# Optimization experiments

Hardware: AMD Instinct MI355X
Metric: run time of the kernel (lower is better)

The kernel has to match this reference:

```python
import jax, jax.numpy as jnp
import numpy as np

N, D_TOK, K = 8192, 256, 16


def knn_idx(xyz, k):
    # squared pairwise distances, diagonal excluded (loop=False)
    sq = jnp.sum(xyz * xyz, axis=-1)                      # [N]
    dist = sq[:, None] - 2.0 * (xyz @ xyz.T) + sq[None, :]  # [N,N]
    dist = dist + jnp.eye(xyz.shape[0], dtype=xyz.dtype) * jnp.asarray(1e10, xyz.dtype)
    _, idx = jax.lax.top_k(-dist, k)                      # [N,k] nearest neighbors j for each target i
    return idx


def edgeconv(x, nbr, W1, b1, W2, b2):
    # EdgeConv message: nn(concat(x_i, x_j - x_i)), aggr = max over neighbors
    n, d = x.shape
    k = nbr.shape[1]
    xi = x[:, None, :]                                    # [N,1,D]
    xj = x[nbr]                                           # [N,k,D] gather
    msg = jnp.concatenate([jnp.broadcast_to(xi, (n, k, d)), xj - xi], axis=-1)  # [N,k,2D]
    h = jax.nn.relu(msg @ W1 + b1) @ W2 + b2              # [N,k,token_dim]
    return jnp.max(h, axis=1)                             # [N,token_dim]


def setup_inputs() -> dict:
    key = jax.random.key(0)
    ks = jax.random.split(key, 10)
    d_in = 2 * (D_TOK + 3)
    s1 = 1.0 / np.sqrt(d_in)
    s2 = 1.0 / np.sqrt(D_TOK)
    return {
        "xyz": jax.random.normal(ks[0], (N, 3), dtype=jnp.float32),
        "feat": jax.random.normal(ks[1], (N, D_TOK), dtype=jnp.float32),
        "W1a": jax.random.normal(ks[2], (d_in, D_TOK), dtype=jnp.float32) * s1,
        "b1a": jnp.zeros((D_TOK,), dtype=jnp.float32),
        "W2a": jax.random.normal(ks[3], (D_TOK, D_TOK), dtype=jnp.float32) * s2,
        "b2a": jnp.zeros((D_TOK,), dtype=jnp.float32),
        "W1b": jax.random.normal(ks[4], (d_in, D_TOK), dtype=jnp.float32) * s1,
        "b1b": jnp.zeros((D_TOK,), dtype=jnp.float32),
        "W2b": jax.random.normal(ks[5], (D_TOK, D_TOK), dtype=jnp.float32) * s2,
        "b2b": jnp.zeros((D_TOK,), dtype=jnp.float32),
    }


def reference(xyz, feat, W1a, b1a, W2a, b2a, W1b, b1b, W2b, b2b):
    nbr = knn_idx(xyz, K)                                 # [N,k], built once, reused by both convs
    x = jnp.concatenate([feat, xyz], axis=-1)             # [N, D_TOK+3]
    x = edgeconv(x, nbr, W1a, b1a, W2a, b2a)              # [N, D_TOK]
    x = jnp.concatenate([x, xyz], axis=-1)                # [N, D_TOK+3]
    x = edgeconv(x, nbr, W1b, b1b, W2b, b2b)              # [N, D_TOK]
    return x
```

## Files before the change

kernel.cpp:

```cpp
#include <hip/hip_runtime.h>
#include <cfloat>

#define N_PTS 8192
#define DTOK 256
#define KNN 16

typedef __attribute__((ext_vector_type(8))) short short8;
typedef __attribute__((ext_vector_type(4))) float float4v;

__device__ inline short f2bf(float f) {
  unsigned u = __float_as_uint(f);
  u += 0x7fffu + ((u >> 16) & 1u);
  return (short)(u >> 16);
}
__device__ inline float bf2f(short h) {
  return __uint_as_float(((unsigned)(unsigned short)h) << 16);
}

__global__ __launch_bounds__(256) void knn_prep_kernel(
    const float* __restrict__ xyz, float4* __restrict__ xyz4) {
  const int i = blockIdx.x * 256 + threadIdx.x;
  float x = xyz[3 * i], y = xyz[3 * i + 1], z = xyz[3 * i + 2];
  float sq = __fadd_rn(__fadd_rn(__fmul_rn(x, x), __fmul_rn(y, y)),
                       __fmul_rn(z, z));
  xyz4[i] = make_float4(x, y, z, sq);
}

__device__ inline float cand_dist(const float4 p, float xi, float yi, float zi,
                                  float sqi, int j, int i) {
  const float dot = fmaf(zi, p.z, fmaf(yi, p.y, __fmul_rn(xi, p.x)));
  float d = __fadd_rn(__fsub_rn(sqi, __fmul_rn(2.0f, dot)), p.w);
  if (j == i) d = __fadd_rn(d, 1e10f);
  return d;
}

#define KCH 512
#define NCH (N_PTS / KCH)

__global__ __launch_bounds__(256) void knn_select_kernel(
    const float4* __restrict__ xyz4, int* __restrict__ nbr) {
  __shared__ float4 cs[2][KCH];
  const int tid = threadIdx.x;
  const int lane = tid & 63;
  const int wave = tid >> 6;
  const int i = blockIdx.x * 4 + wave;

  const float4 pi = xyz4[i];
  const float xi = pi.x, yi = pi.y, zi = pi.z, sqi = pi.w;

  float4 p0 = xyz4[tid];
  float4 p1 = xyz4[tid + 256];
  cs[0][tid] = p0;
  cs[0][tid + 256] = p1;
  __syncthreads();

  float lmin0 = FLT_MAX, lmin1 = FLT_MAX;
  for (int c = 0; c < NCH; ++c) {
    const int b = c & 1;
    if (c < NCH - 1) {
      p0 = xyz4[(c + 1) * KCH + tid];
      p1 = xyz4[(c + 1) * KCH + tid + 256];
    }
    const int base = c * KCH;
    #pragma unroll
    for (int s = 0; s < 8; s += 2) {
      const float4 q0 = cs[b][s * 64 + lane];
      const float4 q1 = cs[b][(s + 1) * 64 + lane];
      lmin0 = fminf(lmin0, cand_dist(q0, xi, yi, zi, sqi,
                                     base + s * 64 + lane, i));
      lmin1 = fminf(lmin1, cand_dist(q1, xi, yi, zi, sqi,
                                     base + (s + 1) * 64 + lane, i));
    }
    if (c < NCH - 1) {
      cs[b ^ 1][tid] = p0;
      cs[b ^ 1][tid + 256] = p1;
    }
    __syncthreads();
  }
  const float lmin = fminf(lmin0, lmin1);

  float v = lmin;
  #pragma unroll
  for (int k = 2; k <= 64; k <<= 1) {
    #pragma unroll
    for (int j = k >> 1; j > 0; j >>= 1) {
      const float o = __shfl_xor(v, j, 64);
      const bool up = ((lane & k) == 0);
      const bool lo = ((lane & j) == 0);
      v = (up == lo) ? fminf(v, o) : fmaxf(v, o);
    }
  }
  const float t = __shfl(v, 15, 64);

  float sd = FLT_MAX;
  int sj = 0;
  float s15 = FLT_MAX;

  p0 = xyz4[tid];
  p1 = xyz4[tid + 256];
  cs[0][tid] = p0;
  cs[0][tid + 256] = p1;
  __syncthreads();

  for (int c = 0; c < NCH; ++c) {
    const int b = c & 1;
    if (c < NCH - 1) {
      p0 = xyz4[(c + 1) * KCH + tid];
      p1 = xyz4[(c + 1) * KCH + tid + 256];
    }
    const int cbase = c * KCH;

    float dd[8];
    #pragma unroll
    for (int s = 0; s < 8; ++s) {
      const float4 q = cs[b][s * 64 + lane];
      dd[s] = cand_dist(q, xi, yi, zi, sqi, cbase + s * 64 + lane, i);
    }

    #pragma unroll
    for (int s = 0; s < 8; ++s) {
      unsigned long long m = __ballot((dd[s] < s15) && (dd[s] <= t));
      const int base = cbase + s * 64;
      while (m) {
        const int src = __ffsll(m) - 1;
        m &= m - 1;
        const float dc = __shfl(dd[s], src);
        if (dc < s15) {
          const int jc = base + src;
          const unsigned long long bm = __ballot(sd <= dc) & 0xFFFFull;
          const int pos = (int)__popcll(bm);
          const float pu = __shfl_up(sd, 1);
          const int ju = __shfl_up(sj, 1);
          if (lane < 16) {
            if (lane > pos)        { sd = pu; sj = ju; }
            else if (lane == pos)  { sd = dc; sj = jc; }
          }
          s15 = __shfl(sd, 15);
        }
      }
    }

    if (c < NCH - 1) {
      cs[b ^ 1][tid] = p0;
      cs[b ^ 1][tid + 256] = p1;
    }
    __syncthreads();
  }
  if (lane < 16) nbr[i * KNN + lane] = sj;
}

__global__ __launch_bounds__(256) void convert_w_kernel(
    const float* __restrict__ W1, short* __restrict__ bhi,
    short* __restrict__ blo) {
  const int n = blockIdx.x;
  const int k = threadIdx.x;
  const float v = (n < 256) ? W1[k * DTOK + n]
                            : W1[(259 + k) * DTOK + (n - 256)];
  short h = f2bf(v);
  bhi[n * 256 + k] = h;
  blo[n * 256 + k] = f2bf(v - bf2f(h));
}

__global__ __launch_bounds__(256, 2) void pq_gemm_fused_kernel(
    const float* __restrict__ A, const short* __restrict__ Bthi,
    const short* __restrict__ Btlo, const float* __restrict__ xyz,
    const float* __restrict__ W1, const float* __restrict__ b1,
    float* __restrict__ R, float* __restrict__ Q) {
  __shared__ short Ahi[64][32], Alo[64][32];
  __shared__ short Bhi[128][32], Blo[128][32];
  __shared__ float Qs[64][65];
  __shared__ float sx[64][3];
  __shared__ float swz[6][64];
  __shared__ float sb1[64];

  const int tid = threadIdx.x;
  const int lane = tid & 63;
  const int wave = tid >> 6;
  const int l15 = lane & 15;
  const int quad = lane >> 4;
  const int mh = wave & 1;
  const int qh = wave >> 1;
  const int m0 = blockIdx.x * 64;
  const int np0 = blockIdx.y * 64;

  if (tid < 64) {
    sx[tid][0] = xyz[(m0 + tid) * 3];
    sx[tid][1] = xyz[(m0 + tid) * 3 + 1];
    sx[tid][2] = xyz[(m0 + tid) * 3 + 2];
  } else if (tid < 128) {
    int n = tid - 64;
    sb1[n] = b1[np0 + n];
    #pragma unroll
    for (int r = 0; r < 3; ++r) {
      swz[r][n] = W1[(256 + r) * DTOK + np0 + n];
      swz[3 + r][n] = W1[(515 + r) * DTOK + np0 + n];
    }
  }

  float4v acc[2][4];
  #pragma unroll
  for (int mf = 0; mf < 2; ++mf)
    #pragma unroll
    for (int nf = 0; nf < 4; ++nf)
      #pragma unroll
      for (int e = 0; e < 4; ++e) acc[mf][nf][e] = 0.f;

  const int ar = tid >> 2;
  const int ak = (tid & 3) * 8;

  #pragma unroll 1
  for (int kc = 0; kc < 8; ++kc) {
    const int k0 = kc * 32;
    __syncthreads();
    {
      const float* asrc = A + (size_t)(m0 + ar) * 256 + k0 + ak;
      float4 a0 = *(const float4*)asrc;
      float4 a1 = *(const float4*)(asrc + 4);
      float v[8] = {a0.x, a0.y, a0.z, a0.w, a1.x, a1.y, a1.z, a1.w};
      short8 h8, l8;
      #pragma unroll
      for (int e = 0; e < 8; ++e) {
        short h = f2bf(v[e]);
        h8[e] = h;
        l8[e] = f2bf(v[e] - bf2f(h));
      }
      *(short8*)(&Ahi[ar][ak]) = h8;
      *(short8*)(&Alo[ar][ak]) = l8;
    }
    #pragma unroll
    for (int l = 0; l < 4; ++l) {
      const int rem = tid + 256 * (l & 1);
      const int row = rem >> 2;
      const int koff = (rem & 3) * 8;
      const int n = (row < 64) ? (np0 + row) : (256 + np0 + row - 64);
      const short* src = ((l < 2) ? Bthi : Btlo) + (size_t)n * 256 + k0 + koff;
      short8 vv = *(const short8*)src;
      if (l < 2) *(short8*)(&Bhi[row][koff]) = vv;
      else       *(short8*)(&Blo[row][koff]) = vv;
    }
    __syncthreads();

    short8 ah[2], al[2], bh[4], bl[4];
    #pragma unroll
    for (int mf = 0; mf < 2; ++mf) {
      ah[mf] = *(const short8*)(&Ahi[mh * 32 + mf * 16 + l15][quad * 8]);
      al[mf] = *(const short8*)(&Alo[mh * 32 + mf * 16 + l15][quad * 8]);
    }
    #pragma unroll
    for (int nf = 0; nf < 4; ++nf) {
      bh[nf] = *(const short8*)(&Bhi[qh * 64 + nf * 16 + l15][quad * 8]);
      bl[nf] = *(const short8*)(&Blo[qh * 64 + nf * 16 + l15][quad * 8]);
    }
    #pragma unroll
    for (int mf = 0; mf < 2; ++mf)
      #pragma unroll
      for (int nf = 0; nf < 4; ++nf) {
        acc[mf][nf] = __builtin_amdgcn_mfma_f32_16x16x32_bf16(
            ah[mf], bh[nf], acc[mf][nf], 0, 0, 0);
        acc[mf][nf] = __builtin_amdgcn_mfma_f32_16x16x32_bf16(
            ah[mf], bl[nf], acc[mf][nf], 0, 0, 0);
        acc[mf][nf] = __builtin_amdgcn_mfma_f32_16x16x32_bf16(
            al[mf], bh[nf], acc[mf][nf], 0, 0, 0);
      }
  }

  if (qh == 1) {
    #pragma unroll
    for (int mf = 0; mf < 2; ++mf)
      #pragma unroll
      for (int nf = 0; nf < 4; ++nf)
        #pragma unroll
        for (int e = 0; e < 4; ++e) {
          int row = mh * 32 + mf * 16 + quad * 4 + e;
          int col = nf * 16 + l15;
          float q = acc[mf][nf][e] + sx[row][0] * swz[3][col] +
                    sx[row][1] * swz[4][col] + sx[row][2] * swz[5][col];
          Qs[row][col] = q;
          Q[(size_t)(m0 + row) * DTOK + np0 + col] = q;
        }
  }
  __syncthreads();
  if (qh == 0) {
    #pragma unroll
    for (int mf = 0; mf < 2; ++mf)
      #pragma unroll
      for (int nf = 0; nf < 4; ++nf)
        #pragma unroll
        for (int e = 0; e < 4; ++e) {
          int row = mh * 32 + mf * 16 + quad * 4 + e;
          int col = nf * 16 + l15;
          float p = acc[mf][nf][e] + sx[row][0] * swz[0][col] +
                    sx[row][1] * swz[1][col] + sx[row][2] * swz[2][col];
          R[(size_t)(m0 + row) * DTOK + np0 + col] =
              (p + sb1[col]) - Qs[row][col];
        }
  }
}

#define EP 8

__global__ __launch_bounds__(256, 2) void edge_mfma_kernel(
    const float* __restrict__ R, const float* __restrict__ Q,
    const int* __restrict__ nbr, const float* __restrict__ W2,
    const float* __restrict__ b2, float* __restrict__ out,
    int num_groups, int groups_per_block) {
  __shared__ short Hs[EP * KNN * DTOK];
  const int lane = threadIdx.x & 63;
  const int wave = threadIdx.x >> 6;
  const int l15 = lane & 15;
  const int quad = lane >> 4;

  short8 bfr[4][8];
  #pragma unroll
  for (int nt_i = 0; nt_i < 4; ++nt_i) {
    const int n = (wave * 4 + nt_i) * 16 + l15;
    #pragma unroll
    for (int kt = 0; kt < 8; ++kt) {
      short8 f;
      #pragma unroll
      for (int jj = 0; jj < 8; ++jj) {
        int k = kt * 32 + quad * 8 + jj;
        f[jj] = f2bf(W2[k * DTOK + n]);
      }
      bfr[nt_i][kt] = f;
    }
  }

  const int wc8 = lane >> 1;
  const int wsub = (lane & 1) * 4;

  for (int gi = 0; gi < groups_per_block; ++gi) {
    const int g = blockIdx.x + gi * gridDim.x;
    if (g >= num_groups) break;
    const int i0 = g * EP;

    {
      const int ia = i0 + wave * 2;
      const int jr0 = nbr[ia * KNN + l15];
      const int jr1 = nbr[(ia + 1) * KNN + l15];
      const float4 ri0 = ((const float4*)(R + (size_t)ia * DTOK))[lane];
      const float4 ri1 = ((const float4*)(R + (size_t)(ia + 1) * DTOK))[lane];
      #pragma unroll
      for (int pp = 0; pp < 2; ++pp) {
        const float4 ri = pp ? ri1 : ri0;
        const int jr = pp ? jr1 : jr0;
        #pragma unroll
        for (int k = 0; k < KNN; ++k) {
          const int j = __shfl(jr, k, 16);
          const float4 qj = ((const float4*)(Q + (size_t)j * DTOK))[lane];
          const int r = wave * 32 + pp * 16 + k;
          uint2 pk;
          pk.x = ((unsigned)(unsigned short)f2bf(fmaxf(ri.x + qj.x, 0.f))) |
                 (((unsigned)(unsigned short)f2bf(fmaxf(ri.y + qj.y, 0.f))) << 16);
          pk.y = ((unsigned)(unsigned short)f2bf(fmaxf(ri.z + qj.z, 0.f))) |
                 (((unsigned)(unsigned short)f2bf(fmaxf(ri.w + qj.w, 0.f))) << 16);
          *(uint2*)(&Hs[r * DTOK + ((wc8 ^ (r & 7)) << 3) + wsub]) = pk;
        }
      }
    }
    __syncthreads();

    #pragma unroll
    for (int mp = 0; mp < 4; ++mp) {
      float4v acc[2][4];
      #pragma unroll
      for (int mi = 0; mi < 2; ++mi)
        #pragma unroll
        for (int nt_i = 0; nt_i < 4; ++nt_i)
          #pragma unroll
          for (int e = 0; e < 4; ++e) acc[mi][nt_i][e] = 0.f;

      #pragma unroll
      for (int kt = 0; kt < 8; ++kt) {
        const int pc = ((kt * 4 + quad) ^ (l15 & 7)) << 3;
        const short8 a0 = *(const short8*)(
            &Hs[((mp * 2 + 0) * 16 + l15) * DTOK + pc]);
        const short8 a1 = *(const short8*)(
            &Hs[((mp * 2 + 1) * 16 + l15) * DTOK + pc]);
        #pragma unroll
        for (int nt_i = 0; nt_i < 4; ++nt_i) {
          acc[0][nt_i] = __builtin_amdgcn_mfma_f32_16x16x32_bf16(
              a0, bfr[nt_i][kt], acc[0][nt_i], 0, 0, 0);
          acc[1][nt_i] = __builtin_amdgcn_mfma_f32_16x16x32_bf16(
              a1, bfr[nt_i][kt], acc[1][nt_i], 0, 0, 0);
        }
      }

      #pragma unroll
      for (int mi = 0; mi < 2; ++mi) {
        #pragma unroll
        for (int nt_i = 0; nt_i < 4; ++nt_i) {
          float rm = fmaxf(fmaxf(acc[mi][nt_i][0], acc[mi][nt_i][1]),
                           fmaxf(acc[mi][nt_i][2], acc[mi][nt_i][3]));
          rm = fmaxf(rm, __shfl_xor(rm, 16, 64));
          rm = fmaxf(rm, __shfl_xor(rm, 32, 64));
          if (lane < 16) {
            const int i = i0 + mp * 2 + mi;
            const int n = (wave * 4 + nt_i) * 16 + lane;
            out[(size_t)i * DTOK + n] = rm + b2[n];
          }
        }
      }
    }
    __syncthreads();
  }
}

extern "C" void kernel_launch(void* const* d_in, const int* in_sizes, int n_in,
                              void* d_out, int out_size, void* d_ws,
                              size_t ws_size, hipStream_t stream) {
  const float* xyz = (const float*)d_in[0];
  const float* feat = (const float*)d_in[1];
  const float* W1a = (const float*)d_in[2];
  const float* b1a = (const float*)d_in[3];
  const float* W2a = (const float*)d_in[4];
  const float* b2a = (const float*)d_in[5];
  const float* W1b = (const float*)d_in[6];
  const float* b1b = (const float*)d_in[7];
  const float* W2b = (const float*)d_in[8];
  const float* b2b = (const float*)d_in[9];
  float* out = (float*)d_out;

  char* w = (char*)d_ws;
  const size_t SZ_NBR = (size_t)N_PTS * KNN * sizeof(int);
  const size_t MB = 1024 * 1024;
  int* nbr = (int*)w;
  char* w1 = w + SZ_NBR;
  float4* xyz4 = (float4*)w1;
  float* R = (float*)(w1 + 8 * MB);
  float* Q = (float*)(w + SZ_NBR + 16 * MB);
  short* Bthi = (short*)(w + SZ_NBR + 24 * MB);
  short* Btlo = Bthi + 512 * 256;
  float* bufC = out;

  knn_prep_kernel<<<N_PTS / 256, 256, 0, stream>>>(xyz, xyz4);
  knn_select_kernel<<<N_PTS / 4, 256, 0, stream>>>(xyz4, nbr);

  const int num_groups = N_PTS / EP;
  const int nblocks = 512;

  convert_w_kernel<<<512, 256, 0, stream>>>(W1a, Bthi, Btlo);
  pq_gemm_fused_kernel<<<dim3(N_PTS / 64, 4), 256, 0, stream>>>(
      feat, Bthi, Btlo, xyz, W1a, b1a, R, Q);
  edge_mfma_kernel<<<nblocks, 256, 0, stream>>>(R, Q, nbr, W2a, b2a, bufC,
                                                num_groups, 2);

  convert_w_kernel<<<512, 256, 0, stream>>>(W1b, Bthi, Btlo);
  pq_gemm_fused_kernel<<<dim3(N_PTS / 64, 4), 256, 0, stream>>>(
      bufC, Bthi, Btlo, xyz, W1b, b1b, R, Q);
  edge_mfma_kernel<<<nblocks, 256, 0, stream>>>(R, Q, nbr, W2b, b2b, out,
                                                num_groups, 2);
}
```

Measured before the change: 240.2 us.

## Use packed FP32 math with SoA shared layout in KNN distance scan

Rearranges the candidate points in shared memory into paired structure-of-arrays (x0,x1,y0,y1 / z0,z1,w0,w1) so each lane computes two distances at once with v_pk_fma/v_pk_mul/v_pk_add inline asm. The self-exclusion test moves from a per-candidate compare to one check per 128-point chunk. In the selection pass the ballot drops its s15 precheck and filters only on d <= t, relying on the inner dc < s15 test. This is meant to halve the VALU instruction count of the distance computation. In exchange, more ballot iterations may run, and the inline asm limits compiler scheduling.

```diff
diff --git a/kernel.cpp b/kernel.cpp
--- a/kernel.cpp
+++ b/kernel.cpp
@@ -7,6 +7,7 @@
 
 typedef __attribute__((ext_vector_type(8))) short short8;
 typedef __attribute__((ext_vector_type(4))) float float4v;
+typedef __attribute__((ext_vector_type(2))) float float2v;
 
 __device__ inline short f2bf(float f) {
   unsigned u = __float_as_uint(f);
@@ -15,6 +16,28 @@
 }
 __device__ inline float bf2f(short h) {
   return __uint_as_float(((unsigned)(unsigned short)h) << 16);
+}
+
+__device__ inline float2v pk_mul(float2v a, float2v b) {
+  float2v d;
+  asm("v_pk_mul_f32 %0, %1, %2" : "=v"(d) : "v"(a), "v"(b));
+  return d;
+}
+__device__ inline float2v pk_fma(float2v a, float2v b, float2v c) {
+  float2v d;
+  asm("v_pk_fma_f32 %0, %1, %2, %3" : "=v"(d) : "v"(a), "v"(b), "v"(c));
+  return d;
+}
+__device__ inline float2v pk_add(float2v a, float2v b) {
+  float2v d;
+  asm("v_pk_add_f32 %0, %1, %2" : "=v"(d) : "v"(a), "v"(b));
+  return d;
+}
+__device__ inline float2v pk_sub(float2v a, float2v b) {
+  float2v d;
+  asm("v_pk_add_f32 %0, %1, %2 neg_lo:[0,1] neg_hi:[0,1]"
+      : "=v"(d) : "v"(a), "v"(b));
+  return d;
 }
 
 __global__ __launch_bounds__(256) void knn_prep_kernel(
@@ -26,54 +49,68 @@
   xyz4[i] = make_float4(x, y, z, sq);
 }
 
-__device__ inline float cand_dist(const float4 p, float xi, float yi, float zi,
-                                  float sqi, int j, int i) {
-  const float dot = fmaf(zi, p.z, fmaf(yi, p.y, __fmul_rn(xi, p.x)));
-  float d = __fadd_rn(__fsub_rn(sqi, __fmul_rn(2.0f, dot)), p.w);
-  if (j == i) d = __fadd_rn(d, 1e10f);
-  return d;
-}
-
 #define KCH 512
 #define NCH (N_PTS / KCH)
 
 __global__ __launch_bounds__(256) void knn_select_kernel(
     const float4* __restrict__ xyz4, int* __restrict__ nbr) {
-  __shared__ float4 cs[2][KCH];
+  __shared__ float4 sA[2][4][64];
+  __shared__ float4 sB[2][4][64];
   const int tid = threadIdx.x;
   const int lane = tid & 63;
   const int wave = tid >> 6;
   const int i = blockIdx.x * 4 + wave;
 
   const float4 pi = xyz4[i];
-  const float xi = pi.x, yi = pi.y, zi = pi.z, sqi = pi.w;
-
-  float4 p0 = xyz4[tid];
-  float4 p1 = xyz4[tid + 256];
-  cs[0][tid] = p0;
-  cs[0][tid + 256] = p1;
+  const float2v xi2 = {pi.x, pi.x};
+  const float2v yi2 = {pi.y, pi.y};
+  const float2v zi2 = {pi.z, pi.z};
+  const float2v sqi2 = {pi.w, pi.w};
+  const float2v two2 = {2.0f, 2.0f};
+
+  const int ib128 = i & ~127;
+  const int ihalf = (i >> 6) & 1;
+  const int il = i & 63;
+
+  const int sgj = wave * 128 + lane;
+
+  {
+    const float4 q0 = xyz4[sgj];
+    const float4 q1 = xyz4[sgj + 64];
+    sA[0][wave][lane] = make_float4(q0.x, q1.x, q0.y, q1.y);
+    sB[0][wave][lane] = make_float4(q0.z, q1.z, q0.w, q1.w);
+  }
   __syncthreads();
 
   float lmin0 = FLT_MAX, lmin1 = FLT_MAX;
   for (int c = 0; c < NCH; ++c) {
     const int b = c & 1;
+    float4 n0, n1;
     if (c < NCH - 1) {
-      p0 = xyz4[(c + 1) * KCH + tid];
-      p1 = xyz4[(c + 1) * KCH + tid + 256];
-    }
-    const int base = c * KCH;
-    #pragma unroll
-    for (int s = 0; s < 8; s += 2) {
-      const float4 q0 = cs[b][s * 64 + lane];
-      const float4 q1 = cs[b][(s + 1) * 64 + lane];
-      lmin0 = fminf(lmin0, cand_dist(q0, xi, yi, zi, sqi,
-                                     base + s * 64 + lane, i));
-      lmin1 = fminf(lmin1, cand_dist(q1, xi, yi, zi, sqi,
-                                     base + (s + 1) * 64 + lane, i));
+      n0 = xyz4[(c + 1) * KCH + sgj];
+      n1 = xyz4[(c + 1) * KCH + sgj + 64];
+    }
+    const int cbase = c * KCH;
+    #pragma unroll
+    for (int ps = 0; ps < 4; ++ps) {
+      const float4 a = sA[b][ps][lane];
+      const float4 bb = sB[b][ps][lane];
+      const float2v px = {a.x, a.y}, py = {a.z, a.w};
+      const float2v pz = {bb.x, bb.y}, pw = {bb.z, bb.w};
+      const float2v dot = pk_fma(zi2, pz, pk_fma(yi2, py, pk_mul(xi2, px)));
+      float2v d = pk_add(pk_sub(sqi2, pk_mul(two2, dot)), pw);
+      if (cbase + ps * 128 == ib128) {
+        if (lane == il) {
+          if (ihalf) d.y = __fadd_rn(d.y, 1e10f);
+          else       d.x = __fadd_rn(d.x, 1e10f);
+        }
+      }
+      lmin0 = fminf(lmin0, d.x);
+      lmin1 = fminf(lmin1, d.y);
     }
     if (c < NCH - 1) {
-      cs[b ^ 1][tid] = p0;
-      cs[b ^ 1][tid + 256] = p1;
+      sA[b ^ 1][wave][lane] = make_float4(n0.x, n1.x, n0.y, n1.y);
+      sB[b ^ 1][wave][lane] = make_float4(n0.z, n1.z, n0.w, n1.w);
     }
     __syncthreads();
   }
@@ -96,53 +133,70 @@
   int sj = 0;
   float s15 = FLT_MAX;
 
-  p0 = xyz4[tid];
-  p1 = xyz4[tid + 256];
-  cs[0][tid] = p0;
-  cs[0][tid + 256] = p1;
+  {
+    const float4 q0 = xyz4[sgj];
+    const float4 q1 = xyz4[sgj + 64];
+    sA[0][wave][lane] = make_float4(q0.x, q1.x, q0.y, q1.y);
+    sB[0][wave][lane] = make_float4(q0.z, q1.z, q0.w, q1.w);
+  }
   __syncthreads();
 
   for (int c = 0; c < NCH; ++c) {
     const int b = c & 1;
+    float4 n0, n1;
     if (c < NCH - 1) {
-      p0 = xyz4[(c + 1) * KCH + tid];
-      p1 = xyz4[(c + 1) * KCH + tid + 256];
+      n0 = xyz4[(c + 1) * KCH + sgj];
+      n1 = xyz4[(c + 1) * KCH + sgj + 64];
     }
     const int cbase = c * KCH;
 
-    float dd[8];
-    #pragma unroll
-    for (int s = 0; s < 8; ++s) {
-      const float4 q = cs[b][s * 64 + lane];
-      dd[s] = cand_dist(q, xi, yi, zi, sqi, cbase + s * 64 + lane, i);
-    }
-
-    #pragma unroll
-    for (int s = 0; s < 8; ++s) {
-      unsigned long long m = __ballot((dd[s] < s15) && (dd[s] <= t));
-      const int base = cbase + s * 64;
-      while (m) {
-        const int src = __ffsll(m) - 1;
-        m &= m - 1;
-        const float dc = __shfl(dd[s], src);
-        if (dc < s15) {
-          const int jc = base + src;
-          const unsigned long long bm = __ballot(sd <= dc) & 0xFFFFull;
-          const int pos = (int)__popcll(bm);
-          const float pu = __shfl_up(sd, 1);
-          const int ju = __shfl_up(sj, 1);
-          if (lane < 16) {
-            if (lane > pos)        { sd = pu; sj = ju; }
-            else if (lane == pos)  { sd = dc; sj = jc; }
+    float2v dd[4];
+    #pragma unroll
+    for (int ps = 0; ps < 4; ++ps) {
+      const float4 a = sA[b][ps][lane];
+      const float4 bb = sB[b][ps][lane];
+      const float2v px = {a.x, a.y}, py = {a.z, a.w};
+      const float2v pz = {bb.x, bb.y}, pw = {bb.z, bb.w};
+      const float2v dot = pk_fma(zi2, pz, pk_fma(yi2, py, pk_mul(xi2, px)));
+      dd[ps] = pk_add(pk_sub(sqi2, pk_mul(two2, dot)), pw);
+      if (cbase + ps * 128 == ib128) {
+        if (lane == il) {
+          if (ihalf) dd[ps].y = __fadd_rn(dd[ps].y, 1e10f);
+          else       dd[ps].x = __fadd_rn(dd[ps].x, 1e10f);
+        }
+      }
+    }
+
+    #pragma unroll
+    for (int ps = 0; ps < 4; ++ps) {
+      #pragma unroll
+      for (int h = 0; h < 2; ++h) {
+        const float d = h ? dd[ps].y : dd[ps].x;
+        const int base = cbase + ps * 128 + h * 64;
+        unsigned long long m = __ballot(d <= t);
+        while (m) {
+          const int src = __ffsll(m) - 1;
+          m &= m - 1;
+          const float dc = __shfl(d, src);
+          if (dc < s15) {
+            const int jc = base + src;
+            const unsigned long long bm = __ballot(sd <= dc) & 0xFFFFull;
+            const int pos = (int)__popcll(bm);
+            const float pu = __shfl_up(sd, 1);
+            const int ju = __shfl_up(sj, 1);
+            if (lane < 16) {
+              if (lane > pos)        { sd = pu; sj = ju; }
+              else if (lane == pos)  { sd = dc; sj = jc; }
+            }
+            s15 = __shfl(sd, 15);
           }
-          s15 = __shfl(sd, 15);
         }
       }
     }
 
     if (c < NCH - 1) {
-      cs[b ^ 1][tid] = p0;
-      cs[b ^ 1][tid + 256] = p1;
+      sA[b ^ 1][wave][lane] = make_float4(n0.x, n1.x, n0.y, n1.y);
+      sB[b ^ 1][wave][lane] = make_float4(n0.z, n1.z, n0.w, n1.w);
     }
     __syncthreads();
   }
```

Result: no change. 239.7 us (-0.2%).
